# Kernel tuning notes

Hardware: AMD Instinct MI355X
Metric: run time of the kernel (lower is better)

The kernel has to match this reference:

```python
import jax, jax.numpy as jnp
import numpy as np

N_NODES = 100000
NEG_SLOPE = 0.2  # PyG GATConv default negative_slope


def gat_layer(x, src, dst, W, a_src, a_dst, b):
    """PyG-style GATConv (eval mode: dropout = identity), concat=True.
    x: [N, F_in]; W: [F_in, H*C]; a_src/a_dst: [H, C]; b: [H*C].
    src/dst: [E] edge endpoints (messages flow src -> dst), self-loops included.
    """
    N = x.shape[0]
    H, C = a_src.shape
    h = (x @ W).reshape(N, H, C)                       # [N, H, C]
    al_s = jnp.sum(h * a_src, axis=-1)                 # [N, H]
    al_d = jnp.sum(h * a_dst, axis=-1)                 # [N, H]
    e = jax.nn.leaky_relu(al_s[src] + al_d[dst], NEG_SLOPE)  # [E, H]
    # softmax over incoming edges of each dst node (every node has a self-loop)
    m = jax.ops.segment_max(e, dst, num_segments=N)    # [N, H]
    ex = jnp.exp(e - m[dst])
    s = jax.ops.segment_sum(ex, dst, num_segments=N)   # [N, H]
    alpha = ex / s[dst]                                # [E, H]
    out = jax.ops.segment_sum(h[src] * alpha[:, :, None], dst, num_segments=N)
    return out.reshape(N, H * C) + b


def setup_inputs() -> dict:
    key = jax.random.key(0)
    ks = jax.random.split(key, 12)
    F_in, Hc, H, n_cls = 128, 32, 4, 3
    x = jax.random.normal(ks[0], (N_NODES, F_in), dtype=jnp.float32)
    edge_index = jax.random.randint(ks[1], (2, 1600000), 0, N_NODES, dtype=jnp.int64)
    sc1 = 1.0 / np.sqrt(F_in)
    sc2 = 1.0 / np.sqrt(Hc * H)
    return {
        "x": x,
        "edge_index": edge_index,
        "W1": jax.random.normal(ks[2], (F_in, H * Hc), dtype=jnp.float32) * sc1,
        "a1_src": jax.random.normal(ks[3], (H, Hc), dtype=jnp.float32) * sc1,
        "a1_dst": jax.random.normal(ks[4], (H, Hc), dtype=jnp.float32) * sc1,
        "b1": jnp.zeros((H * Hc,), dtype=jnp.float32),
        "W2": jax.random.normal(ks[5], (H * Hc, Hc), dtype=jnp.float32) * sc2,
        "a2_src": jax.random.normal(ks[6], (1, Hc), dtype=jnp.float32) * sc2,
        "a2_dst": jax.random.normal(ks[7], (1, Hc), dtype=jnp.float32) * sc2,
        "b2": jnp.zeros((Hc,), dtype=jnp.float32),
        "lin_W": jax.random.normal(ks[8], (Hc, n_cls), dtype=jnp.float32) * (1.0 / np.sqrt(Hc)),
        "lin_b": jnp.zeros((n_cls,), dtype=jnp.float32),
    }


def reference(x, edge_index, W1, a1_src, a1_dst, b1, W2, a2_src, a2_dst, b2, lin_W, lin_b):
    N = x.shape[0]
    loops = jnp.arange(N, dtype=edge_index.dtype)
    src = jnp.concatenate([edge_index[0], loops])
    dst = jnp.concatenate([edge_index[1], loops])
    h = jax.nn.elu(gat_layer(x, src, dst, W1, a1_src, a1_dst, b1))
    h = gat_layer(h, src, dst, W2, a2_src, a2_dst, b2)
    pooled = h.mean(axis=0, keepdims=True)             # batch=None path: [1, Hc]
    return jax.nn.softmax(pooled @ lin_W + lin_b, axis=1)
```

## Files before the change

kernel.cpp:

```cpp
#include <hip/hip_runtime.h>
#include <cstdint>
#include <cstddef>

static inline size_t align_up(size_t v, size_t a) { return (v + a - 1) & ~(a - 1); }

#define BCAP 3072

typedef __attribute__((ext_vector_type(8))) short short8;
typedef __attribute__((ext_vector_type(4))) float f32x4;
typedef __attribute__((ext_vector_type(2))) float f32x2;

__device__ inline unsigned short bf16_1(float x) {
  unsigned u = __float_as_uint(x);
  u += 0x7FFFu + ((u >> 16) & 1u);
  return (unsigned short)(u >> 16);
}
__device__ inline unsigned cvt_pk_bf16(float lo, float hi) {
  unsigned r;
  asm("v_cvt_pk_bf16_f32 %0, %1, %2" : "=v"(r) : "v"(lo), "v"(hi));
  return r;
}

__device__ inline unsigned char fp8_1(float x) {
  return (unsigned char)(__builtin_amdgcn_cvt_pk_fp8_f32(x, x, 0, false) & 0xFF);
}

__global__ void prep_kernel(const float* __restrict__ W1, const float* __restrict__ W2,
                            unsigned short* __restrict__ w1t, unsigned short* __restrict__ w2t,
                            int* __restrict__ fillB) {
  int t = blockIdx.x * 256 + threadIdx.x;
  if (t < 16384) {
    int c = t >> 7, k = t & 127;
    w1t[t] = bf16_1(W1[(size_t)k * 128 + c]);
  } else if (t < 20480) {
    int i = t - 16384;
    int c = i >> 7, k = i & 127;
    w2t[i] = bf16_1(W2[(size_t)k * 32 + c]);
  } else if (t < 21504) {
    fillB[t - 20480] = 0;
  }
}

__device__ inline int load_edge(const void* eidx, int is64, size_t idx) {
  if (is64) return (int)((const long long*)eidx)[idx];
  return ((const int*)eidx)[idx];
}


__device__ void sortA_body(char* smem, const void* eidx, int E,
                           int* __restrict__ fillB, unsigned* __restrict__ packed,
                           int NB, int bid) {
  int* hist = (int*)smem;
  int* loff = hist + 1024;
  int* lbase = loff + 1024;
  int* lcnt = lbase + 1024;
  unsigned* sortedV = (unsigned*)(lcnt + 1024);
  unsigned short* sortedB = (unsigned short*)(sortedV + 2048);
  int* sd = (int*)(sortedB + 2048);
  int* s_is64 = sd + 256;
  const int t = threadIdx.x;
  const int chunk0 = bid * 2048;
  const int cntE = min(2048, E - chunk0);
  if (t == 0) *s_is64 = 1;
  for (int i = t; i < 1024; i += 256) { hist[i] = 0; lcnt[i] = 0; }
  __syncthreads();
  {
    int nchk = min(cntE, 256);
    for (int i = t; i < nchk; i += 256)
      if (((const unsigned*)eidx)[2 * (size_t)(chunk0 + i) + 1] != 0u) *s_is64 = 0;
  }
  __syncthreads();
  const int is64 = *s_is64;
  int sv[8], dv[8];
#pragma unroll
  for (int it = 0; it < 8; ++it) {
    int li = it * 256 + t;
    if (li < cntE) {
      sv[it] = load_edge(eidx, is64, (size_t)chunk0 + li);
      dv[it] = load_edge(eidx, is64, (size_t)E + chunk0 + li);
      atomicAdd(&hist[dv[it] >> 7], 1);
    }
  }
  __syncthreads();
  for (int b = t; b < NB; b += 256) {
    int h = hist[b];
    if (h) lbase[b] = b * BCAP + atomicAdd(&fillB[b], h);
  }
  {
    int base = t * 4;
    int v[4]; int s = 0;
#pragma unroll
    for (int j = 0; j < 4; ++j) { v[j] = hist[base + j]; s += v[j]; }
    sd[t] = s; __syncthreads();
    for (int off = 1; off < 256; off <<= 1) {
      int u = (t >= off) ? sd[t - off] : 0;
      __syncthreads();
      sd[t] += u;
      __syncthreads();
    }
    int run = sd[t] - s;
#pragma unroll
    for (int j = 0; j < 4; ++j) { loff[base + j] = run; run += v[j]; }
  }
  __syncthreads();
#pragma unroll
  for (int it = 0; it < 8; ++it) {
    int li = it * 256 + t;
    if (li < cntE) {
      int b = dv[it] >> 7;
      int r = atomicAdd(&lcnt[b], 1);
      int pos = loff[b] + r;
      sortedV[pos] = (unsigned)sv[it] | ((unsigned)(dv[it] & 127) << 20);
      sortedB[pos] = (unsigned short)b;
    }
  }
  __syncthreads();
  for (int li = t; li < cntE; li += 256) {
    int b = sortedB[li];
    packed[(size_t)lbase[b] + (li - loff[b])] = sortedV[li];
  }
}

__device__ void gemm1_body(char* smem,
    const float* __restrict__ x, const unsigned short* __restrict__ w1t,
    const float* __restrict__ a1s, const float* __restrict__ a1d,
    unsigned char* __restrict__ h1f, float* __restrict__ al1s, float* __restrict__ al1d,
    int N, int bid) {
  unsigned short* sw = (unsigned short*)smem;
  unsigned short* sx = sw + 128 * 136;
  unsigned char* ftile = (unsigned char*)sx;
  const int t = threadIdx.x;
  const int row0 = bid * 64;
  for (int i = t; i < 4096; i += 256) {
    int c = i >> 5, k4 = (i & 31) * 4;
    *(ushort4*)&sw[c * 136 + k4] = *(const ushort4*)&w1t[c * 128 + k4];
  }
  for (int i = t; i < 2048; i += 256) {
    int r = i >> 5, c4 = (i & 31) * 4;
    float4 v = make_float4(0.f, 0.f, 0.f, 0.f);
    if (row0 + r < N) v = *(const float4*)(x + (size_t)(row0 + r) * 128 + c4);
    uint2 b;
    b.x = cvt_pk_bf16(v.x, v.y);
    b.y = cvt_pk_bf16(v.z, v.w);
    *(uint2*)&sx[r * 136 + c4] = b;
  }
  __syncthreads();
  const int lane = t & 63, wave = t >> 6;
  const int m = lane & 15, quad = lane >> 4;
  const unsigned short* arow = &sx[(wave * 16 + m) * 136];
  short8 A[4];
#pragma unroll
  for (int ks = 0; ks < 4; ++ks) A[ks] = *(const short8*)&arow[ks * 32 + quad * 8];
  __syncthreads();
  const int lrow = wave * 16 + quad * 4;
#pragma unroll
  for (int nt = 0; nt < 8; ++nt) {
    const unsigned short* brow = &sw[(nt * 16 + m) * 136];
    f32x4 acc = {0.f, 0.f, 0.f, 0.f};
#pragma unroll
    for (int ks = 0; ks < 4; ++ks) {
      short8 B = *(const short8*)&brow[ks * 32 + quad * 8];
      acc = __builtin_amdgcn_mfma_f32_16x16x32_bf16(A[ks], B, acc, 0, 0, 0);
    }
#pragma unroll
    for (int r = 0; r < 4; ++r)
      ftile[(lrow + r) * 128 + nt * 16 + m] = fp8_1(acc[r]);
  }
  __syncthreads();
#pragma unroll
  for (int it = 0; it < 2; ++it) {
    int row = it * 32 + (t >> 3);
    int chunk = t & 7;
    uint4 v = *(const uint4*)&ftile[row * 128 + chunk * 16];
    int grow = row0 + row;
    if (grow < N) *(uint4*)&h1f[(size_t)grow * 128 + chunk * 16] = v;
    unsigned w[4] = {v.x, v.y, v.z, v.w};
    float ps = 0.f, pd = 0.f;
    int cb = chunk * 16;
#pragma unroll
    for (int q = 0; q < 4; ++q) {
      f32x2 lo = __builtin_amdgcn_cvt_pk_f32_fp8((int)w[q], false);
      f32x2 hi = __builtin_amdgcn_cvt_pk_f32_fp8((int)w[q], true);
      int c = cb + q * 4;
      ps += lo[0] * a1s[c] + lo[1] * a1s[c + 1] + hi[0] * a1s[c + 2] + hi[1] * a1s[c + 3];
      pd += lo[0] * a1d[c] + lo[1] * a1d[c + 1] + hi[0] * a1d[c + 2] + hi[1] * a1d[c + 3];
    }
    ps += __shfl_xor(ps, 1); pd += __shfl_xor(pd, 1);
    if ((chunk & 1) == 0 && grow < N) {
      int head = chunk >> 1;
      al1s[(size_t)grow * 4 + head] = ps;
      al1d[(size_t)grow * 4 + head] = pd;
    }
  }
}

__global__ __launch_bounds__(256) void fused_sort_gemm1(
    const void* eidx, int E, int* __restrict__ fillB, unsigned* __restrict__ packed,
    int NB, int NBs,
    const float* __restrict__ x, const unsigned short* __restrict__ w1t,
    const float* __restrict__ a1s, const float* __restrict__ a1d,
    unsigned char* __restrict__ h1f, float* __restrict__ al1s, float* __restrict__ al1d,
    int N) {
  __shared__ __align__(16) char smem[52224];
  int bid = blockIdx.x;
  if (bid < NBs) {
    sortA_body(smem, eidx, E, fillB, packed, NB, bid);
  } else {
    gemm1_body(smem, x, w1t, a1s, a1d, h1f, al1s, al1d, N, bid - NBs);
  }
}

__global__ __launch_bounds__(256) void buildCSR_kernel(const unsigned* __restrict__ packed,
                                                       const int* __restrict__ fillB,
                                                       int* __restrict__ rowbeg,
                                                       int* __restrict__ rowend,
                                                       int* __restrict__ csr, int N, int NB) {
  __shared__ int cnt[128], ex[128], fill[128];
  const int b = blockIdx.x;
  const int t = threadIdx.x;
  const int beg = b * BCAP;
  const int end = beg + fillB[b];
  const int node0 = b << 7;
  const int nn = min(128, N - node0);
  if (t < 128) { cnt[t] = 0; fill[t] = 0; }
  __syncthreads();
  for (int i = beg + t; i < end; i += 256) {
    int j = (packed[i] >> 20) & 127;
    atomicAdd(&cnt[j], 1);
  }
  __syncthreads();
  if (t < 128) ex[t] = cnt[t];
  __syncthreads();
  for (int off = 1; off < 128; off <<= 1) {
    int u = (t >= off && t < 128) ? ex[t - off] : 0;
    __syncthreads();
    if (t < 128) ex[t] += u;
    __syncthreads();
  }
  if (t < 128) ex[t] -= cnt[t];
  __syncthreads();
  if (t < nn) {
    rowbeg[node0 + t] = beg + ex[t];
    rowend[node0 + t] = beg + ex[t] + cnt[t];
  }
  for (int i = beg + t; i < end; i += 256) {
    unsigned v = packed[i];
    int j = (v >> 20) & 127;
    int r = atomicAdd(&fill[j], 1);
    csr[beg + ex[j] + r] = (int)(v & 0xFFFFFu);
  }
}

__global__ __launch_bounds__(256) void gemm2_mfma(
    const unsigned* __restrict__ houtb, const unsigned short* __restrict__ w2t,
    const float* __restrict__ a2s, const float* __restrict__ a2d,
    unsigned char* __restrict__ h2f, float* __restrict__ al2s, float* __restrict__ al2d, int N) {
  __shared__ unsigned short sw[32 * 136];
  __shared__ unsigned short sx[64 * 136];
  unsigned char* ftile = (unsigned char*)sx;
  const int t = threadIdx.x;
  const int row0 = blockIdx.x * 64;
  for (int i = t; i < 1024; i += 256) {
    int c = i >> 5, k4 = (i & 31) * 4;
    *(ushort4*)&sw[c * 136 + k4] = *(const ushort4*)&w2t[c * 128 + k4];
  }
  for (int i = t; i < 2048; i += 256) {
    int r = i >> 5, d2 = (i & 31) * 2;
    uint2 v = make_uint2(0u, 0u);
    if (row0 + r < N) v = *(const uint2*)(houtb + (size_t)(row0 + r) * 64 + d2);
    *(uint2*)&sx[r * 136 + d2 * 2] = v;
  }
  __syncthreads();
  const int lane = t & 63, wave = t >> 6;
  const int m = lane & 15, quad = lane >> 4;
  const unsigned short* arow = &sx[(wave * 16 + m) * 136];
  short8 A[4];
#pragma unroll
  for (int ks = 0; ks < 4; ++ks) A[ks] = *(const short8*)&arow[ks * 32 + quad * 8];
  __syncthreads();
  const int lrow = wave * 16 + quad * 4;
#pragma unroll
  for (int nt = 0; nt < 2; ++nt) {
    const unsigned short* brow = &sw[(nt * 16 + m) * 136];
    f32x4 acc = {0.f, 0.f, 0.f, 0.f};
#pragma unroll
    for (int ks = 0; ks < 4; ++ks) {
      short8 B = *(const short8*)&brow[ks * 32 + quad * 8];
      acc = __builtin_amdgcn_mfma_f32_16x16x32_bf16(A[ks], B, acc, 0, 0, 0);
    }
#pragma unroll
    for (int r = 0; r < 4; ++r)
      ftile[(lrow + r) * 32 + nt * 16 + m] = fp8_1(acc[r]);
  }
  __syncthreads();
  if (t < 128) {
    int row = t >> 1, chunk = t & 1;
    uint4 v = *(const uint4*)&ftile[row * 32 + chunk * 16];
    int grow = row0 + row;
    if (grow < N) *(uint4*)&h2f[(size_t)grow * 32 + chunk * 16] = v;
    unsigned w[4] = {v.x, v.y, v.z, v.w};
    float ps = 0.f, pd = 0.f;
    int cb = chunk * 16;
#pragma unroll
    for (int q = 0; q < 4; ++q) {
      f32x2 lo = __builtin_amdgcn_cvt_pk_f32_fp8((int)w[q], false);
      f32x2 hi = __builtin_amdgcn_cvt_pk_f32_fp8((int)w[q], true);
      int c = cb + q * 4;
      ps += lo[0] * a2s[c] + lo[1] * a2s[c + 1] + hi[0] * a2s[c + 2] + hi[1] * a2s[c + 3];
      pd += lo[0] * a2d[c] + lo[1] * a2d[c + 1] + hi[0] * a2d[c + 2] + hi[1] * a2d[c + 3];
    }
    ps += __shfl_xor(ps, 1); pd += __shfl_xor(pd, 1);
    if (chunk == 0 && grow < N) { al2s[grow] = ps; al2d[grow] = pd; }
  }
}

#define DEC8P(HV, EX)                                                       \
  {                                                                         \
    f32x2 _e2; _e2[0] = (EX); _e2[1] = (EX);                                \
    acc01 += __builtin_amdgcn_cvt_pk_f32_fp8((int)(HV).x, false) * _e2;     \
    acc23 += __builtin_amdgcn_cvt_pk_f32_fp8((int)(HV).x, true) * _e2;      \
    acc45 += __builtin_amdgcn_cvt_pk_f32_fp8((int)(HV).y, false) * _e2;     \
    acc67 += __builtin_amdgcn_cvt_pk_f32_fp8((int)(HV).y, true) * _e2;      \
    den += (EX);                                                            \
  }

__global__ __launch_bounds__(256) void agg1_kernel(
    const int* __restrict__ rowbeg, const int* __restrict__ rowend, const int* __restrict__ csr_src,
    const unsigned char* __restrict__ h1f,
    const float* __restrict__ al_s, const float* __restrict__ al_d,
    const float* __restrict__ b1, unsigned* __restrict__ houtb, int N) {
  int t = threadIdx.x;
  int d = (blockIdx.x * 256 + t) >> 6;
  if (d >= N) return;
  int lane = t & 63;
  int e_id = lane >> 4;
  unsigned c8 = (unsigned)(lane & 15);
  unsigned head = c8 >> 2;
  const unsigned boff = c8 * 8u;
  const float ald = al_d[(unsigned)d * 4u + head];
  const int beg = __builtin_amdgcn_readfirstlane(rowbeg[d]);
  const int end = __builtin_amdgcn_readfirstlane(rowend[d]);
  int idx0 = beg + e_id;
  int idx1 = idx0 + 4;
  int sj0 = (idx0 < end) ? csr_src[(unsigned)idx0] : d;
  int sj1 = (idx1 < end) ? csr_src[(unsigned)idx1] : d;
  f32x2 acc01 = {0.f, 0.f}, acc23 = {0.f, 0.f}, acc45 = {0.f, 0.f}, acc67 = {0.f, 0.f};
  float den = 0.f;
  {
    float e = al_s[(unsigned)d * 4u + head] + ald;
    e = fmaxf(e, 0.2f * e);
    float ex = (e_id == 0) ? __expf(e) : 0.f;
    uint2 hv = *(const uint2*)(h1f + (((unsigned)d << 7) | boff));
    DEC8P(hv, ex);
  }
  for (int i = beg; i < end; i += 8) {
    const int cidx0 = idx0, cidx1 = idx1;
    const int csj0 = sj0, csj1 = sj1;
    float as0 = al_s[(unsigned)csj0 * 4u + head];
    float as1 = al_s[(unsigned)csj1 * 4u + head];
    uint2 hv0 = *(const uint2*)(h1f + (((unsigned)csj0 << 7) | boff));
    uint2 hv1 = *(const uint2*)(h1f + (((unsigned)csj1 << 7) | boff));
    idx0 += 8; idx1 += 8;
    sj0 = (idx0 < end) ? csr_src[(unsigned)idx0] : d;
    sj1 = (idx1 < end) ? csr_src[(unsigned)idx1] : d;
    float e0 = as0 + ald;
    e0 = fmaxf(e0, 0.2f * e0);
    float ex0 = __expf(e0);
    if (cidx0 >= end) ex0 = 0.f;
    float e1 = as1 + ald;
    e1 = fmaxf(e1, 0.2f * e1);
    float ex1 = __expf(e1);
    if (cidx1 >= end) ex1 = 0.f;
    DEC8P(hv0, ex0);
    DEC8P(hv1, ex1);
  }
  float a0 = acc01[0], a1 = acc01[1], a2 = acc23[0], a3 = acc23[1];
  float a4 = acc45[0], a5 = acc45[1], a6 = acc67[0], a7 = acc67[1];
  a0 += __shfl_xor(a0, 16); a1 += __shfl_xor(a1, 16);
  a2 += __shfl_xor(a2, 16); a3 += __shfl_xor(a3, 16);
  a4 += __shfl_xor(a4, 16); a5 += __shfl_xor(a5, 16);
  a6 += __shfl_xor(a6, 16); a7 += __shfl_xor(a7, 16);
  den += __shfl_xor(den, 16);
  a0 += __shfl_xor(a0, 32); a1 += __shfl_xor(a1, 32);
  a2 += __shfl_xor(a2, 32); a3 += __shfl_xor(a3, 32);
  a4 += __shfl_xor(a4, 32); a5 += __shfl_xor(a5, 32);
  a6 += __shfl_xor(a6, 32); a7 += __shfl_xor(a7, 32);
  den += __shfl_xor(den, 32);
  float inv = __builtin_amdgcn_rcpf(den);
  float p0 = e_id == 0 ? a0 : e_id == 1 ? a2 : e_id == 2 ? a4 : a6;
  float p1 = e_id == 0 ? a1 : e_id == 1 ? a3 : e_id == 2 ? a5 : a7;
  float2 bv = *(const float2*)(b1 + 8 * c8 + 2 * e_id);
  float o0 = p0 * inv + bv.x;
  float o1 = p1 * inv + bv.y;
  o0 = o0 > 0.f ? o0 : __expf(o0) - 1.f;
  o1 = o1 > 0.f ? o1 : __expf(o1) - 1.f;
  houtb[(unsigned)d * 64u + 4u * c8 + (unsigned)e_id] = cvt_pk_bf16(o0, o1);
}

__global__ __launch_bounds__(256) void agg2_kernel(
    const int* __restrict__ rowbeg, const int* __restrict__ rowend, const int* __restrict__ csr_src,
    const unsigned char* __restrict__ h2f,
    const float* __restrict__ al_s, const float* __restrict__ al_d,
    float* __restrict__ partial, int N) {
  __shared__ float sp[16 * 32];
  int t = threadIdx.x;
  int l16 = t & 15;
  int slot = t >> 4;
  int node = (blockIdx.x * 256 + t) >> 4;
  int e_id = l16 >> 2;
  unsigned c8 = (unsigned)(l16 & 3);
  const unsigned boff = c8 * 8u;
  float po0 = 0.f, po1 = 0.f;
  if (node < N) {
    const float ald = al_d[node];
    const int beg = rowbeg[node], end = rowend[node];
    int idx0 = beg + e_id;
    int idx1 = idx0 + 4;
    int sj0 = (idx0 < end) ? csr_src[(unsigned)idx0] : node;
    int sj1 = (idx1 < end) ? csr_src[(unsigned)idx1] : node;
    float self_as = al_s[node];
    uint2 self_hv = *(const uint2*)(h2f + (((unsigned)node << 5) | boff));
    idx0 += 8; idx1 += 8;
    int nsj0 = (idx0 < end) ? csr_src[(unsigned)idx0] : node;
    int nsj1 = (idx1 < end) ? csr_src[(unsigned)idx1] : node;
    float as0 = al_s[(unsigned)sj0];
    float as1 = al_s[(unsigned)sj1];
    uint2 hv0 = *(const uint2*)(h2f + (((unsigned)sj0 << 5) | boff));
    uint2 hv1 = *(const uint2*)(h2f + (((unsigned)sj1 << 5) | boff));
    f32x2 acc01 = {0.f, 0.f}, acc23 = {0.f, 0.f}, acc45 = {0.f, 0.f}, acc67 = {0.f, 0.f};
    float den = 0.f;
    {
      float e = self_as + ald;
      e = fmaxf(e, 0.2f * e);
      float ex = (e_id == 0) ? __expf(e) : 0.f;
      DEC8P(self_hv, ex);
    }
    for (int i = beg; i < end; i += 8) {
      idx0 += 8; idx1 += 8;
      int nnsj0 = (idx0 < end) ? csr_src[(unsigned)idx0] : node;
      int nnsj1 = (idx1 < end) ? csr_src[(unsigned)idx1] : node;
      float nas0 = al_s[(unsigned)nsj0];
      float nas1 = al_s[(unsigned)nsj1];
      uint2 nhv0 = *(const uint2*)(h2f + (((unsigned)nsj0 << 5) | boff));
      uint2 nhv1 = *(const uint2*)(h2f + (((unsigned)nsj1 << 5) | boff));
      int cix0 = i + e_id;
      int cix1 = cix0 + 4;
      float e0 = as0 + ald;
      e0 = fmaxf(e0, 0.2f * e0);
      float ex0 = __expf(e0);
      if (cix0 >= end) ex0 = 0.f;
      float e1 = as1 + ald;
      e1 = fmaxf(e1, 0.2f * e1);
      float ex1 = __expf(e1);
      if (cix1 >= end) ex1 = 0.f;
      DEC8P(hv0, ex0);
      DEC8P(hv1, ex1);
      as0 = nas0; as1 = nas1; hv0 = nhv0; hv1 = nhv1;
      nsj0 = nnsj0; nsj1 = nnsj1;
    }
    float a0 = acc01[0], a1 = acc01[1], a2 = acc23[0], a3 = acc23[1];
    float a4 = acc45[0], a5 = acc45[1], a6 = acc67[0], a7 = acc67[1];
    a0 += __shfl_xor(a0, 4); a1 += __shfl_xor(a1, 4);
    a2 += __shfl_xor(a2, 4); a3 += __shfl_xor(a3, 4);
    a4 += __shfl_xor(a4, 4); a5 += __shfl_xor(a5, 4);
    a6 += __shfl_xor(a6, 4); a7 += __shfl_xor(a7, 4);
    den += __shfl_xor(den, 4);
    a0 += __shfl_xor(a0, 8); a1 += __shfl_xor(a1, 8);
    a2 += __shfl_xor(a2, 8); a3 += __shfl_xor(a3, 8);
    a4 += __shfl_xor(a4, 8); a5 += __shfl_xor(a5, 8);
    a6 += __shfl_xor(a6, 8); a7 += __shfl_xor(a7, 8);
    den += __shfl_xor(den, 8);
    float inv = __builtin_amdgcn_rcpf(den);
    float p0 = e_id == 0 ? a0 : e_id == 1 ? a2 : e_id == 2 ? a4 : a6;
    float p1 = e_id == 0 ? a1 : e_id == 1 ? a3 : e_id == 2 ? a5 : a7;
    po0 = p0 * inv; po1 = p1 * inv;
  }
  *(float2*)&sp[slot * 32 + 8 * c8 + 2 * e_id] = make_float2(po0, po1);
  __syncthreads();
  if (t < 32) {
    float s = 0.f;
#pragma unroll
    for (int j = 0; j < 16; ++j) s += sp[j * 32 + t];
    partial[(size_t)blockIdx.x * 32 + t] = s;
  }
}

__global__ __launch_bounds__(256) void reduce_kernel(
    const float* __restrict__ partial, int nb, float* __restrict__ partial2) {
  __shared__ float sp[8 * 32];
  int t = threadIdx.x;
  int slot = t >> 5, c = t & 31;
  int row0 = blockIdx.x * 8 + slot;
  float s = 0.f;
  for (int i = row0; i < nb; i += 1024) s += partial[(size_t)i * 32 + c];
  sp[slot * 32 + c] = s;
  __syncthreads();
  if (t < 32) {
    float tot = 0.f;
#pragma unroll
    for (int j = 0; j < 8; ++j) tot += sp[j * 32 + t];
    partial2[(size_t)blockIdx.x * 32 + t] = tot;
  }
}

__global__ void final_kernel(const float* __restrict__ partial2, int nb,
                             const float* __restrict__ b2, const float* __restrict__ linW,
                             const float* __restrict__ linb, float* __restrict__ out, int N) {
  __shared__ float sd[256];
  __shared__ float pooled[32];
  int t = threadIdx.x;
  int c = t & 31, g = t >> 5;
  float s = 0.f;
  for (int i = g; i < nb; i += 8) s += partial2[(size_t)i * 32 + c];
  sd[t] = s; __syncthreads();
  if (t < 32) {
    float tot = 0.f;
#pragma unroll
    for (int j = 0; j < 8; ++j) tot += sd[j * 32 + t];
    pooled[t] = tot / (float)N + b2[t];
  }
  __syncthreads();
  if (t == 0) {
    float lg[3];
    for (int j = 0; j < 3; ++j) lg[j] = linb[j];
    for (int cc = 0; cc < 32; ++cc)
      for (int j = 0; j < 3; ++j) lg[j] += pooled[cc] * linW[cc * 3 + j];
    float m = fmaxf(lg[0], fmaxf(lg[1], lg[2]));
    float e0 = __expf(lg[0] - m), e1 = __expf(lg[1] - m), e2 = __expf(lg[2] - m);
    float inv = 1.f / (e0 + e1 + e2);
    out[0] = e0 * inv; out[1] = e1 * inv; out[2] = e2 * inv;
  }
}

extern "C" void kernel_launch(void* const* d_in, const int* in_sizes, int n_in,
                              void* d_out, int out_size, void* d_ws, size_t ws_size,
                              hipStream_t stream) {
  const float* x    = (const float*)d_in[0];
  const void*  eidx = d_in[1];
  const float* W1   = (const float*)d_in[2];
  const float* a1s  = (const float*)d_in[3];
  const float* a1d  = (const float*)d_in[4];
  const float* b1   = (const float*)d_in[5];
  const float* W2   = (const float*)d_in[6];
  const float* a2s  = (const float*)d_in[7];
  const float* a2d  = (const float*)d_in[8];
  const float* b2   = (const float*)d_in[9];
  const float* linW = (const float*)d_in[10];
  const float* linb = (const float*)d_in[11];
  float* out = (float*)d_out;

  const int N = in_sizes[0] / 128;
  const int E = in_sizes[1] / 2;
  const int NB = (N + 127) >> 7;

  char* ws = (char*)d_ws;
  size_t off = 0;
  auto alloc = [&](size_t bytes) -> void* {
    size_t o = off;
    off = align_up(off + bytes, 256);
    return (void*)(ws + o);
  };
  int* fillB  = (int*)alloc((size_t)1024 * sizeof(int));
  int* rowbeg = (int*)alloc((size_t)N * sizeof(int));
  int* rowend = (int*)alloc((size_t)N * sizeof(int));
  unsigned* packed = (unsigned*)alloc((size_t)NB * BCAP * sizeof(unsigned));
  int* csr    = (int*)alloc((size_t)NB * BCAP * sizeof(int));
  float* al1s = (float*)alloc((size_t)N * 4 * sizeof(float));
  float* al1d = (float*)alloc((size_t)N * 4 * sizeof(float));
  float* al2s = (float*)alloc((size_t)N * sizeof(float));
  float* al2d = (float*)alloc((size_t)N * sizeof(float));
  unsigned short* w1t = (unsigned short*)alloc(16384 * sizeof(unsigned short));
  unsigned short* w2t = (unsigned short*)alloc(4096 * sizeof(unsigned short));
  unsigned char* h1f  = (unsigned char*)alloc((size_t)N * 128);
  unsigned* houtb = (unsigned*)alloc((size_t)N * 64 * sizeof(unsigned));
  unsigned char* h2f  = (unsigned char*)alloc((size_t)N * 32);
  const int nAggBlocks = (N + 15) / 16;
  float* partial  = (float*)alloc((size_t)nAggBlocks * 32 * sizeof(float));
  float* partial2 = (float*)alloc((size_t)128 * 32 * sizeof(float));

  prep_kernel<<<84, 256, 0, stream>>>(W1, W2, w1t, w2t, fillB);

  const int NBs = (E + 2047) / 2048;
  const int gemmBlocks = (N + 63) / 64;
  fused_sort_gemm1<<<NBs + gemmBlocks, 256, 0, stream>>>(
      eidx, E, fillB, packed, NB, NBs, x, w1t, a1s, a1d, h1f, al1s, al1d, N);

  buildCSR_kernel<<<NB, 256, 0, stream>>>(packed, fillB, rowbeg, rowend, csr, N, NB);
  agg1_kernel<<<(N * 64 + 255) / 256, 256, 0, stream>>>(
      rowbeg, rowend, csr, h1f, al1s, al1d, b1, houtb, N);
  gemm2_mfma<<<gemmBlocks, 256, 0, stream>>>(houtb, w2t, a2s, a2d, h2f, al2s, al2d, N);
  agg2_kernel<<<(N * 16 + 255) / 256, 256, 0, stream>>>(
      rowbeg, rowend, csr, h2f, al2s, al2d, partial, N);
  reduce_kernel<<<128, 256, 0, stream>>>(partial, nAggBlocks, partial2);
  final_kernel<<<1, 256, 0, stream>>>(partial2, 128, b2, linW, linb, out, N);
}
```

Before: 261.2 us.

## Replace two-pass bucket sort CSR build with per-node histogram and atomic scatter

Replaces the bucketed two-level sort (per-chunk local sort into 128-node buckets, then a per-bucket CSR build) with a direct counting sort. It does a global per-node atomic histogram fused with gemm1, a per-bucket prefix scan that writes row offsets, and then an atomic scatter of source indices into the CSR. This drops the packed intermediate buffer and the shared-memory sorting work. In exchange it adds many global atomics on per-node counters, reads the edge list twice, and writes the CSR in random order.

```diff
diff --git a/kernel.cpp b/kernel.cpp
--- a/kernel.cpp
+++ b/kernel.cpp
@@ -27,7 +27,7 @@
 
 __global__ void prep_kernel(const float* __restrict__ W1, const float* __restrict__ W2,
                             unsigned short* __restrict__ w1t, unsigned short* __restrict__ w2t,
-                            int* __restrict__ fillB) {
+                            int* __restrict__ cnt, int N) {
   int t = blockIdx.x * 256 + threadIdx.x;
   if (t < 16384) {
     int c = t >> 7, k = t & 127;
@@ -36,9 +36,8 @@
     int i = t - 16384;
     int c = i >> 7, k = i & 127;
     w2t[i] = bf16_1(W2[(size_t)k * 32 + c]);
-  } else if (t < 21504) {
-    fillB[t - 20480] = 0;
-  }
+  }
+  for (int i = t; i < N; i += gridDim.x * 256) cnt[i] = 0;
 }
 
 __device__ inline int load_edge(const void* eidx, int is64, size_t idx) {
@@ -47,22 +46,12 @@
 }
 
 
-__device__ void sortA_body(char* smem, const void* eidx, int E,
-                           int* __restrict__ fillB, unsigned* __restrict__ packed,
-                           int NB, int bid) {
-  int* hist = (int*)smem;
-  int* loff = hist + 1024;
-  int* lbase = loff + 1024;
-  int* lcnt = lbase + 1024;
-  unsigned* sortedV = (unsigned*)(lcnt + 1024);
-  unsigned short* sortedB = (unsigned short*)(sortedV + 2048);
-  int* sd = (int*)(sortedB + 2048);
-  int* s_is64 = sd + 256;
+__device__ void hist_body(int* s_is64, const void* eidx, int E,
+                          int* __restrict__ cnt, int bid) {
   const int t = threadIdx.x;
-  const int chunk0 = bid * 2048;
-  const int cntE = min(2048, E - chunk0);
+  const int chunk0 = bid * 4096;
+  const int cntE = min(4096, E - chunk0);
   if (t == 0) *s_is64 = 1;
-  for (int i = t; i < 1024; i += 256) { hist[i] = 0; lcnt[i] = 0; }
   __syncthreads();
   {
     int nchk = min(cntE, 256);
@@ -71,53 +60,13 @@
   }
   __syncthreads();
   const int is64 = *s_is64;
-  int sv[8], dv[8];
-#pragma unroll
-  for (int it = 0; it < 8; ++it) {
-    int li = it * 256 + t;
+#pragma unroll
+  for (int k = 0; k < 16; ++k) {
+    int li = k * 256 + t;
     if (li < cntE) {
-      sv[it] = load_edge(eidx, is64, (size_t)chunk0 + li);
-      dv[it] = load_edge(eidx, is64, (size_t)E + chunk0 + li);
-      atomicAdd(&hist[dv[it] >> 7], 1);
-    }
-  }
-  __syncthreads();
-  for (int b = t; b < NB; b += 256) {
-    int h = hist[b];
-    if (h) lbase[b] = b * BCAP + atomicAdd(&fillB[b], h);
-  }
-  {
-    int base = t * 4;
-    int v[4]; int s = 0;
-#pragma unroll
-    for (int j = 0; j < 4; ++j) { v[j] = hist[base + j]; s += v[j]; }
-    sd[t] = s; __syncthreads();
-    for (int off = 1; off < 256; off <<= 1) {
-      int u = (t >= off) ? sd[t - off] : 0;
-      __syncthreads();
-      sd[t] += u;
-      __syncthreads();
-    }
-    int run = sd[t] - s;
-#pragma unroll
-    for (int j = 0; j < 4; ++j) { loff[base + j] = run; run += v[j]; }
-  }
-  __syncthreads();
-#pragma unroll
-  for (int it = 0; it < 8; ++it) {
-    int li = it * 256 + t;
-    if (li < cntE) {
-      int b = dv[it] >> 7;
-      int r = atomicAdd(&lcnt[b], 1);
-      int pos = loff[b] + r;
-      sortedV[pos] = (unsigned)sv[it] | ((unsigned)(dv[it] & 127) << 20);
-      sortedB[pos] = (unsigned short)b;
-    }
-  }
-  __syncthreads();
-  for (int li = t; li < cntE; li += 256) {
-    int b = sortedB[li];
-    packed[(size_t)lbase[b] + (li - loff[b])] = sortedV[li];
+      int dv = load_edge(eidx, is64, (size_t)E + chunk0 + li);
+      atomicAdd(&cnt[dv], 1);
+    }
   }
 }
 
@@ -194,60 +143,70 @@
   }
 }
 
-__global__ __launch_bounds__(256) void fused_sort_gemm1(
-    const void* eidx, int E, int* __restrict__ fillB, unsigned* __restrict__ packed,
-    int NB, int NBs,
+__global__ __launch_bounds__(256) void fused_hist_gemm1(
+    const void* eidx, int E, int* __restrict__ cnt, int NHB,
     const float* __restrict__ x, const unsigned short* __restrict__ w1t,
     const float* __restrict__ a1s, const float* __restrict__ a1d,
     unsigned char* __restrict__ h1f, float* __restrict__ al1s, float* __restrict__ al1d,
     int N) {
   __shared__ __align__(16) char smem[52224];
   int bid = blockIdx.x;
-  if (bid < NBs) {
-    sortA_body(smem, eidx, E, fillB, packed, NB, bid);
+  if (bid < NHB) {
+    hist_body((int*)smem, eidx, E, cnt, bid);
   } else {
-    gemm1_body(smem, x, w1t, a1s, a1d, h1f, al1s, al1d, N, bid - NBs);
-  }
-}
-
-__global__ __launch_bounds__(256) void buildCSR_kernel(const unsigned* __restrict__ packed,
-                                                       const int* __restrict__ fillB,
+    gemm1_body(smem, x, w1t, a1s, a1d, h1f, al1s, al1d, N, bid - NHB);
+  }
+}
+
+__global__ __launch_bounds__(128) void buildRow_kernel(int* __restrict__ cntfill,
                                                        int* __restrict__ rowbeg,
-                                                       int* __restrict__ rowend,
-                                                       int* __restrict__ csr, int N, int NB) {
-  __shared__ int cnt[128], ex[128], fill[128];
-  const int b = blockIdx.x;
-  const int t = threadIdx.x;
-  const int beg = b * BCAP;
-  const int end = beg + fillB[b];
+                                                       int* __restrict__ rowend, int N) {
+  __shared__ int ex[128];
+  const int b = blockIdx.x, t = threadIdx.x;
   const int node0 = b << 7;
   const int nn = min(128, N - node0);
-  if (t < 128) { cnt[t] = 0; fill[t] = 0; }
-  __syncthreads();
-  for (int i = beg + t; i < end; i += 256) {
-    int j = (packed[i] >> 20) & 127;
-    atomicAdd(&cnt[j], 1);
-  }
-  __syncthreads();
-  if (t < 128) ex[t] = cnt[t];
+  int c = (t < nn) ? cntfill[node0 + t] : 0;
+  ex[t] = c;
   __syncthreads();
   for (int off = 1; off < 128; off <<= 1) {
-    int u = (t >= off && t < 128) ? ex[t - off] : 0;
+    int u = (t >= off) ? ex[t - off] : 0;
     __syncthreads();
-    if (t < 128) ex[t] += u;
+    ex[t] += u;
     __syncthreads();
   }
-  if (t < 128) ex[t] -= cnt[t];
-  __syncthreads();
+  int rb = b * BCAP + ex[t] - c;
   if (t < nn) {
-    rowbeg[node0 + t] = beg + ex[t];
-    rowend[node0 + t] = beg + ex[t] + cnt[t];
-  }
-  for (int i = beg + t; i < end; i += 256) {
-    unsigned v = packed[i];
-    int j = (v >> 20) & 127;
-    int r = atomicAdd(&fill[j], 1);
-    csr[beg + ex[j] + r] = (int)(v & 0xFFFFFu);
+    rowbeg[node0 + t] = rb;
+    rowend[node0 + t] = rb + c;
+    cntfill[node0 + t] = rb;
+  }
+}
+
+__global__ __launch_bounds__(256) void scatter_kernel(const void* eidx, int E,
+                                                      int* __restrict__ fillp,
+                                                      int* __restrict__ csr) {
+  __shared__ int s_is64;
+  const int t = threadIdx.x;
+  const int chunk0 = blockIdx.x * 2048;
+  const int cntE = min(2048, E - chunk0);
+  if (t == 0) s_is64 = 1;
+  __syncthreads();
+  {
+    int nchk = min(cntE, 256);
+    for (int i = t; i < nchk; i += 256)
+      if (((const unsigned*)eidx)[2 * (size_t)(chunk0 + i) + 1] != 0u) s_is64 = 0;
+  }
+  __syncthreads();
+  const int is64 = s_is64;
+#pragma unroll
+  for (int k = 0; k < 8; ++k) {
+    int li = k * 256 + t;
+    if (li < cntE) {
+      int sv = load_edge(eidx, is64, (size_t)chunk0 + li);
+      int dv = load_edge(eidx, is64, (size_t)E + chunk0 + li);
+      int pos = atomicAdd(&fillp[dv], 1);
+      csr[pos] = sv;
+    }
   }
 }
 
@@ -560,10 +519,9 @@
     off = align_up(off + bytes, 256);
     return (void*)(ws + o);
   };
-  int* fillB  = (int*)alloc((size_t)1024 * sizeof(int));
+  int* cnt    = (int*)alloc((size_t)N * sizeof(int));
   int* rowbeg = (int*)alloc((size_t)N * sizeof(int));
   int* rowend = (int*)alloc((size_t)N * sizeof(int));
-  unsigned* packed = (unsigned*)alloc((size_t)NB * BCAP * sizeof(unsigned));
   int* csr    = (int*)alloc((size_t)NB * BCAP * sizeof(int));
   float* al1s = (float*)alloc((size_t)N * 4 * sizeof(float));
   float* al1d = (float*)alloc((size_t)N * 4 * sizeof(float));
@@ -578,14 +536,16 @@
   float* partial  = (float*)alloc((size_t)nAggBlocks * 32 * sizeof(float));
   float* partial2 = (float*)alloc((size_t)128 * 32 * sizeof(float));
 
-  prep_kernel<<<84, 256, 0, stream>>>(W1, W2, w1t, w2t, fillB);
-
-  const int NBs = (E + 2047) / 2048;
+  prep_kernel<<<84, 256, 0, stream>>>(W1, W2, w1t, w2t, cnt, N);
+
+  const int NHB = (E + 4095) / 4096;
   const int gemmBlocks = (N + 63) / 64;
-  fused_sort_gemm1<<<NBs + gemmBlocks, 256, 0, stream>>>(
-      eidx, E, fillB, packed, NB, NBs, x, w1t, a1s, a1d, h1f, al1s, al1d, N);
-
-  buildCSR_kernel<<<NB, 256, 0, stream>>>(packed, fillB, rowbeg, rowend, csr, N, NB);
+  fused_hist_gemm1<<<NHB + gemmBlocks, 256, 0, stream>>>(
+      eidx, E, cnt, NHB, x, w1t, a1s, a1d, h1f, al1s, al1d, N);
+
+  buildRow_kernel<<<NB, 128, 0, stream>>>(cnt, rowbeg, rowend, N);
+  scatter_kernel<<<(E + 2047) / 2048, 256, 0, stream>>>(eidx, E, cnt, csr);
+
   agg1_kernel<<<(N * 64 + 255) / 256, 256, 0, stream>>>(
       rowbeg, rowend, csr, h1f, al1s, al1d, b1, houtb, N);
   gemm2_mfma<<<gemmBlocks, 256, 0, stream>>>(houtb, w2t, a2s, a2d, h2f, al2s, al2d, N);
```

Result: slower. 416.5 us (+59.4%).
